# Optimization experiments

Measured on AMD Instinct MI355X. Metric: run time of the kernel, lower is better.

Reference implementation:

```python
import jax, jax.numpy as jnp
import numpy as np
from jax import lax

NB_ITER = 10
HALF = 1
ALPHA = 0.2


def setup_inputs() -> dict:
    key = jax.random.key(0)
    k1, = jax.random.split(key, 1)
    B, C, H, W = 16, 64, 256, 256
    o = jax.random.normal(k1, (B, C, H, W), dtype=jnp.float32)
    nb_sigma = 5.0 * jnp.ones((C, 1, 1), dtype=jnp.float32)  # matches init [5.0]*C
    lam = jnp.ones((1,), dtype=jnp.float32)                   # matches init [1.0]
    return {"o": o, "nb_sigma": nb_sigma, "lam": lam}


def _std_kernel(nb_sigma):
    # nb_sigma: (C,1,1) -> kernel (C,1,k,k) with k = 2*HALF+1
    coords = jnp.arange(-HALF, HALF + 1, dtype=jnp.float32)
    x, y = jnp.meshgrid(coords, coords, indexing="ij")
    r2 = x ** 2 + y ** 2  # (k,k)
    sig2 = nb_sigma * nb_sigma  # (C,1,1)
    ker = jnp.exp(-r2 / (2.0 * sig2)) / (0.2 * jnp.pi * sig2)  # (C,k,k)
    return ker[:, None, :, :]  # (C,1,k,k) depthwise OIHW


def _leaky(x):
    return jnp.where(x >= 0, x, ALPHA * x)


def reference(o, nb_sigma, lam):
    C = o.shape[1]
    ker = _std_kernel(nb_sigma)
    u = _leaky(o)
    lam_s = lam[0]
    for _ in range(NB_ITER):
        q = lax.conv_general_dilated(
            1.0 - 2.0 * u, ker,
            window_strides=(1, 1),
            padding=[(HALF, HALF), (HALF, HALF)],
            dimension_numbers=("NCHW", "OIHW", "NCHW"),
            feature_group_count=C,
        )
        u = _leaky(o - lam_s * q)
    return u
```

## Files before the change

kernel.cpp:

```cpp
#include <hip/hip_runtime.h>

#define ALPHA 0.2f

__device__ __forceinline__ float dpp_up1(float x) {
  return __builtin_bit_cast(float, __builtin_amdgcn_update_dpp(
      0, __builtin_bit_cast(int, x), 0x138, 0xf, 0xf, true));
}
__device__ __forceinline__ float dpp_dn1(float x) {
  return __builtin_bit_cast(float, __builtin_amdgcn_update_dpp(
      0, __builtin_bit_cast(int, x), 0x130, 0xf, 0xf, true));
}

__device__ __forceinline__ float leaky_f(float x) { return fmaxf(x, ALPHA * x); }

__global__ __launch_bounds__(64, 2) void pipe_k(
    const float* __restrict__ o,
    const float* __restrict__ nb_sigma,
    const float* __restrict__ lam,
    float* __restrict__ out)
{
  __shared__ float ring[12][256];

  const int lane  = threadIdx.x;
  const int x4    = lane << 2;
  const int bid   = blockIdx.x;
  const int strip = bid & 1;
  const int plane = bid >> 1;
  const int c     = plane & 63;
  const int y0    = strip << 7;
  const int start = y0 - 10;

  const float sig  = nb_sigma[c];
  const float sig2 = sig * sig;
  const float w1   = expf(-0.5f / sig2);
  const float s    = lam[0] / (0.62831853071795864769f * sig2);

  const float* __restrict__ pb = o   + ((size_t)plane << 16);
  float* __restrict__       ob = out + ((size_t)plane << 16);

  float4 v[10][3];
#pragma unroll
  for (int k = 0; k < 10; ++k)
#pragma unroll
    for (int j = 0; j < 3; ++j)
      v[k][j] = make_float4(0.f, 0.f, 0.f, 0.f);

  auto ldrow = [&](int r) -> float4 {
    int rr = r < 0 ? 0 : (r > 255 ? 255 : r);
    return *reinterpret_cast<const float4*>(pb + (rr << 8) + x4);
  };

  float4 ocur  = ldrow(start);
  float4 onext = ldrow(start + 1);
  int bslot = 0;

#pragma unroll 1
  for (int it = 0; it < 50; ++it) {
#pragma unroll
    for (int p = 0; p < 3; ++p) {
      const int t = it * 3 + p;
      const int r = start + t;

      float4 onn = ldrow(r + 2);

      *reinterpret_cast<float4*>(&ring[bslot][x4]) = ocur;

      float4 v0;
      if (r >= 0 && r <= 255) {
        v0.x = fmaf(-2.f, leaky_f(ocur.x), 1.f);
        v0.y = fmaf(-2.f, leaky_f(ocur.y), 1.f);
        v0.z = fmaf(-2.f, leaky_f(ocur.z), 1.f);
        v0.w = fmaf(-2.f, leaky_f(ocur.w), 1.f);
      } else {
        v0 = make_float4(0.f, 0.f, 0.f, 0.f);
      }
      v[0][p] = v0;

#pragma unroll
      for (int k = 1; k <= 10; ++k) {
        const int rho = r - k;
        const float4 a  = v[k-1][(p + 1) % 3];
        const float4 b  = v[k-1][(p + 2) % 3];
        const float4 cc = v[k-1][p];

        float4 g;
        g.x = fmaf(w1, a.x + cc.x, b.x);
        g.y = fmaf(w1, a.y + cc.y, b.y);
        g.z = fmaf(w1, a.z + cc.z, b.z);
        g.w = fmaf(w1, a.w + cc.w, b.w);

        const float gl = dpp_up1(g.w);
        const float gr = dpp_dn1(g.x);

        float4 q;
        q.x = fmaf(w1, gl  + g.y, g.x);
        q.y = fmaf(w1, g.x + g.z, g.y);
        q.z = fmaf(w1, g.y + g.w, g.z);
        q.w = fmaf(w1, g.z + gr , g.w);

        int sk = bslot - k; if (sk < 0) sk += 12;
        const float4 ok = *reinterpret_cast<const float4*>(&ring[sk][x4]);

        float4 u;
        { float e = fmaf(-s, q.x, ok.x); u.x = leaky_f(e); }
        { float e = fmaf(-s, q.y, ok.y); u.y = leaky_f(e); }
        { float e = fmaf(-s, q.z, ok.z); u.z = leaky_f(e); }
        { float e = fmaf(-s, q.w, ok.w); u.w = leaky_f(e); }

        if (k < 10) {
          float4 nv;
          if (rho >= 0 && rho <= 255) {
            nv.x = fmaf(-2.f, u.x, 1.f);
            nv.y = fmaf(-2.f, u.y, 1.f);
            nv.z = fmaf(-2.f, u.z, 1.f);
            nv.w = fmaf(-2.f, u.w, 1.f);
          } else {
            nv = make_float4(0.f, 0.f, 0.f, 0.f);
          }
          v[k][p] = nv;
        } else {
          if (rho >= y0 && rho < y0 + 128) {
            __builtin_nontemporal_store(u.x, ob + (rho << 8) + x4 + 0);
            __builtin_nontemporal_store(u.y, ob + (rho << 8) + x4 + 1);
            __builtin_nontemporal_store(u.z, ob + (rho << 8) + x4 + 2);
            __builtin_nontemporal_store(u.w, ob + (rho << 8) + x4 + 3);
          }
        }
      }

      ocur  = onext;
      onext = onn;
      bslot = (bslot == 11) ? 0 : bslot + 1;
    }
  }
}

extern "C" void kernel_launch(void* const* d_in, const int* in_sizes, int n_in,
                              void* d_out, int out_size, void* d_ws, size_t ws_size,
                              hipStream_t stream)
{
  const float* o        = (const float*)d_in[0];
  const float* nb_sigma = (const float*)d_in[1];
  const float* lam      = (const float*)d_in[2];
  float* out = (float*)d_out;

  pipe_k<<<dim3(2048), dim3(64), 0, stream>>>(o, nb_sigma, lam, out);
}
```

Baseline: 488.6 us.

## Restructure separable stencil pipeline with horizontal-first pass and pending vertical accumulators

Reorders the separable 3x3 stencil so the horizontal DPP pass runs first on each new row, and the vertical contribution is spread over two pending accumulators per stage. This replaces the three-row register history per stage and removes the 3-way unrolled phase loop. It also makes the boundary masks branchless and uses a single vector nontemporal store, with waves_per_eu pinned to 2. The rolled 150-iteration loop may add loop overhead and shifts register pressure from 30 to 20 float4 state variables plus extra adds.

```diff
diff --git a/kernel.cpp b/kernel.cpp
--- a/kernel.cpp
+++ b/kernel.cpp
@@ -1,6 +1,8 @@
 #include <hip/hip_runtime.h>
 
 #define ALPHA 0.2f
+
+typedef float f4 __attribute__((ext_vector_type(4)));
 
 __device__ __forceinline__ float dpp_up1(float x) {
   return __builtin_bit_cast(float, __builtin_amdgcn_update_dpp(
@@ -13,7 +15,9 @@
 
 __device__ __forceinline__ float leaky_f(float x) { return fmaxf(x, ALPHA * x); }
 
-__global__ __launch_bounds__(64, 2) void pipe_k(
+__global__ __launch_bounds__(64)
+__attribute__((amdgpu_waves_per_eu(2, 2)))
+void pipe_k(
     const float* __restrict__ o,
     const float* __restrict__ nb_sigma,
     const float* __restrict__ lam,
@@ -38,100 +42,93 @@
   const float* __restrict__ pb = o   + ((size_t)plane << 16);
   float* __restrict__       ob = out + ((size_t)plane << 16);
 
-  float4 v[10][3];
+  f4 pend0[10], pend1[10];
 #pragma unroll
-  for (int k = 0; k < 10; ++k)
-#pragma unroll
-    for (int j = 0; j < 3; ++j)
-      v[k][j] = make_float4(0.f, 0.f, 0.f, 0.f);
+  for (int k = 0; k < 10; ++k) {
+    pend0[k] = (f4)0.0f;
+    pend1[k] = (f4)0.0f;
+  }
 
-  auto ldrow = [&](int r) -> float4 {
+  auto ldrow = [&](int r) -> f4 {
     int rr = r < 0 ? 0 : (r > 255 ? 255 : r);
-    return *reinterpret_cast<const float4*>(pb + (rr << 8) + x4);
+    return *reinterpret_cast<const f4*>(pb + (rr << 8) + x4);
   };
 
-  float4 ocur  = ldrow(start);
-  float4 onext = ldrow(start + 1);
+  f4 ocur  = ldrow(start);
+  f4 onext = ldrow(start + 1);
   int bslot = 0;
 
 #pragma unroll 1
-  for (int it = 0; it < 50; ++it) {
+  for (int t = 0; t < 150; ++t) {
+    const int r = start + t;
+
+    f4 onn = ldrow(r + 2);
+
+    *reinterpret_cast<f4*>(&ring[bslot][x4]) = ocur;
+
+    const bool in0 = (r >= 0) & (r <= 255);
+    const float m0 = in0 ? -2.0f : 0.0f;
+    const float c0 = in0 ?  1.0f : 0.0f;
+    f4 w;
+    w.x = fmaf(m0, leaky_f(ocur.x), c0);
+    w.y = fmaf(m0, leaky_f(ocur.y), c0);
+    w.z = fmaf(m0, leaky_f(ocur.z), c0);
+    w.w = fmaf(m0, leaky_f(ocur.w), c0);
+
+    int sk = bslot;
 #pragma unroll
-    for (int p = 0; p < 3; ++p) {
-      const int t = it * 3 + p;
-      const int r = start + t;
+    for (int k = 1; k <= 10; ++k) {
+      sk = (sk == 0) ? 11 : sk - 1;
 
-      float4 onn = ldrow(r + 2);
+      const float hl = dpp_up1(w.w);
+      const float hr = dpp_dn1(w.x);
+      f4 h;
+      h.x = fmaf(w1, hl  + w.y, w.x);
+      h.y = fmaf(w1, w.x + w.z, w.y);
+      h.z = fmaf(w1, w.y + w.w, w.z);
+      h.w = fmaf(w1, w.z + hr , w.w);
 
-      *reinterpret_cast<float4*>(&ring[bslot][x4]) = ocur;
+      f4 g;
+      g.x = fmaf(w1, h.x, pend0[k-1].x);
+      g.y = fmaf(w1, h.y, pend0[k-1].y);
+      g.z = fmaf(w1, h.z, pend0[k-1].z);
+      g.w = fmaf(w1, h.w, pend0[k-1].w);
+      pend0[k-1].x = pend1[k-1].x + h.x;
+      pend0[k-1].y = pend1[k-1].y + h.y;
+      pend0[k-1].z = pend1[k-1].z + h.z;
+      pend0[k-1].w = pend1[k-1].w + h.w;
+      pend1[k-1].x = w1 * h.x;
+      pend1[k-1].y = w1 * h.y;
+      pend1[k-1].z = w1 * h.z;
+      pend1[k-1].w = w1 * h.w;
 
-      float4 v0;
-      if (r >= 0 && r <= 255) {
-        v0.x = fmaf(-2.f, leaky_f(ocur.x), 1.f);
-        v0.y = fmaf(-2.f, leaky_f(ocur.y), 1.f);
-        v0.z = fmaf(-2.f, leaky_f(ocur.z), 1.f);
-        v0.w = fmaf(-2.f, leaky_f(ocur.w), 1.f);
+      const f4 ok = *reinterpret_cast<const f4*>(&ring[sk][x4]);
+
+      f4 u;
+      u.x = leaky_f(fmaf(-s, g.x, ok.x));
+      u.y = leaky_f(fmaf(-s, g.y, ok.y));
+      u.z = leaky_f(fmaf(-s, g.z, ok.z));
+      u.w = leaky_f(fmaf(-s, g.w, ok.w));
+
+      const int rho = r - k;
+      if (k < 10) {
+        const bool in = (rho >= 0) & (rho <= 255);
+        const float mm = in ? -2.0f : 0.0f;
+        const float cc = in ?  1.0f : 0.0f;
+        w.x = fmaf(mm, u.x, cc);
+        w.y = fmaf(mm, u.y, cc);
+        w.z = fmaf(mm, u.z, cc);
+        w.w = fmaf(mm, u.w, cc);
       } else {
-        v0 = make_float4(0.f, 0.f, 0.f, 0.f);
-      }
-      v[0][p] = v0;
-
-#pragma unroll
-      for (int k = 1; k <= 10; ++k) {
-        const int rho = r - k;
-        const float4 a  = v[k-1][(p + 1) % 3];
-        const float4 b  = v[k-1][(p + 2) % 3];
-        const float4 cc = v[k-1][p];
-
-        float4 g;
-        g.x = fmaf(w1, a.x + cc.x, b.x);
-        g.y = fmaf(w1, a.y + cc.y, b.y);
-        g.z = fmaf(w1, a.z + cc.z, b.z);
-        g.w = fmaf(w1, a.w + cc.w, b.w);
-
-        const float gl = dpp_up1(g.w);
-        const float gr = dpp_dn1(g.x);
-
-        float4 q;
-        q.x = fmaf(w1, gl  + g.y, g.x);
-        q.y = fmaf(w1, g.x + g.z, g.y);
-        q.z = fmaf(w1, g.y + g.w, g.z);
-        q.w = fmaf(w1, g.z + gr , g.w);
-
-        int sk = bslot - k; if (sk < 0) sk += 12;
-        const float4 ok = *reinterpret_cast<const float4*>(&ring[sk][x4]);
-
-        float4 u;
-        { float e = fmaf(-s, q.x, ok.x); u.x = leaky_f(e); }
-        { float e = fmaf(-s, q.y, ok.y); u.y = leaky_f(e); }
-        { float e = fmaf(-s, q.z, ok.z); u.z = leaky_f(e); }
-        { float e = fmaf(-s, q.w, ok.w); u.w = leaky_f(e); }
-
-        if (k < 10) {
-          float4 nv;
-          if (rho >= 0 && rho <= 255) {
-            nv.x = fmaf(-2.f, u.x, 1.f);
-            nv.y = fmaf(-2.f, u.y, 1.f);
-            nv.z = fmaf(-2.f, u.z, 1.f);
-            nv.w = fmaf(-2.f, u.w, 1.f);
-          } else {
-            nv = make_float4(0.f, 0.f, 0.f, 0.f);
-          }
-          v[k][p] = nv;
-        } else {
-          if (rho >= y0 && rho < y0 + 128) {
-            __builtin_nontemporal_store(u.x, ob + (rho << 8) + x4 + 0);
-            __builtin_nontemporal_store(u.y, ob + (rho << 8) + x4 + 1);
-            __builtin_nontemporal_store(u.z, ob + (rho << 8) + x4 + 2);
-            __builtin_nontemporal_store(u.w, ob + (rho << 8) + x4 + 3);
-          }
+        if (rho >= y0 && rho < y0 + 128) {
+          __builtin_nontemporal_store(u, reinterpret_cast<f4*>(ob + (rho << 8) + x4));
         }
       }
+    }
 
-      ocur  = onext;
-      onext = onn;
-      bslot = (bslot == 11) ? 0 : bslot + 1;
-    }
+    ocur  = onext;
+    onext = onn;
+    bslot = (bslot == 11) ? 0 : bslot + 1;
   }
 }
 
```

Measured after the change: 574.4 us. +17.6%, slower.
